# Optimization experiments

Hardware: AMD Instinct MI355X
Metric: run time of the kernel (lower is better)

Reference implementation:

```python
import jax, jax.numpy as jnp
import numpy as np
import math


def pos_enc_3d(h, w, d, c):
    # Faithful PositionalEncoding3D: channels = ceil(c/6)*2 (made even), sin/cos per axis.
    cpe = int(np.ceil(c / 6) * 2)
    if cpe % 2:
        cpe += 1
    inv_freq = 1.0 / (10000.0 ** (np.arange(0, cpe, 2, dtype=np.float32) / cpe))

    def axis_emb(n):
        s = np.arange(n, dtype=np.float32)[:, None] * inv_freq  # (n, cpe//2)
        return np.concatenate([np.sin(s), np.cos(s)], axis=-1)  # (n, cpe)

    ex = np.broadcast_to(axis_emb(h)[:, None, None, :], (h, w, d, cpe))
    ey = np.broadcast_to(axis_emb(w)[None, :, None, :], (h, w, d, cpe))
    ez = np.broadcast_to(axis_emb(d)[None, None, :, :], (h, w, d, cpe))
    emb = np.concatenate([ex, ey, ez], axis=-1)[..., :c]  # (h,w,d,c)
    return jnp.asarray(np.transpose(emb, (3, 0, 1, 2)))  # (c,h,w,d)


def conv3d(x, w, b):
    # x: (b,c,h,w,d), w: (o,i,3,3,3), padding=1
    y = jax.lax.conv_general_dilated(
        x, w, window_strides=(1, 1, 1), padding=[(1, 1)] * 3,
        dimension_numbers=('NCHWD', 'OIHWD', 'NCHWD'))
    return y + b[None, :, None, None, None]


def setup_inputs() -> dict:
    key = jax.random.key(0)
    ks = jax.random.split(key, 12)
    B, C, H, W, D = 2, 64, 16, 16, 16
    C8 = C // 8
    s_emb = 1.0 / math.sqrt(C)
    s_conv = 1.0 / math.sqrt(C * 27)
    return {
        'x': jax.random.normal(ks[0], (B, C, H, W, D), dtype=jnp.float32),
        'Wq': jax.random.normal(ks[1], (C, C), dtype=jnp.float32) * s_emb,
        'Wk': jax.random.normal(ks[2], (C, C), dtype=jnp.float32) * s_emb,
        'Wv': jax.random.normal(ks[3], (C, C), dtype=jnp.float32) * s_emb,
        'qw': jax.random.normal(ks[4], (C8, C, 3, 3, 3), dtype=jnp.float32) * s_conv,
        'qb': jax.random.normal(ks[5], (C8,), dtype=jnp.float32) * 0.01,
        'kw': jax.random.normal(ks[6], (C8, C, 3, 3, 3), dtype=jnp.float32) * s_conv,
        'kb': jax.random.normal(ks[7], (C8,), dtype=jnp.float32) * 0.01,
        'vw': jax.random.normal(ks[8], (C, C, 3, 3, 3), dtype=jnp.float32) * s_conv,
        'vb': jax.random.normal(ks[9], (C,), dtype=jnp.float32) * 0.01,
        'lam1': jax.random.normal(ks[10], (1,), dtype=jnp.float32) * 0.5,
        'lam2': jax.random.normal(ks[11], (1,), dtype=jnp.float32) * 0.5,
    }


def reference(x, Wq, Wk, Wv, qw, qb, kw, kb, vw, vb, lam1, lam2):
    b, c, h, w, d = x.shape
    n = h * w * d
    # NOTE: torch code does `x += pe` in-place inside SelfAttention, so the
    # PE-added x is also what GSA and the residual see.
    pe = pos_enc_3d(h, w, d, c)  # (c,h,w,d)
    x_pe = x + pe[None]

    # ---- SelfAttention (TSA) ----
    tok = x_pe.reshape(b, c, n).transpose(0, 2, 1)  # (b,n,c)
    Q = jnp.einsum('bnc,cd->bnd', tok, Wq)
    K = jnp.einsum('bnc,cd->bnd', tok, Wk)
    V = jnp.einsum('bnc,cd->bnd', tok, Wv)
    A = jax.nn.softmax(jnp.einsum('bic,bjc->bij', Q, K) / math.sqrt(c), axis=-1)
    tsa = jnp.einsum('bij,bjc->bic', A, V).transpose(0, 2, 1).reshape(b, c, h, w, d)

    # ---- GlobalSpatialAttention (GSA) ----
    M = conv3d(x_pe, qw, qb).reshape(b, c // 8, n)   # (b,c/8,n)
    Nk = conv3d(x_pe, kw, kb).reshape(b, c // 8, n)  # (b,c/8,n)
    Wv_ = conv3d(x_pe, vw, vb).reshape(b, c, n)      # (b,c,n)
    Bm = jax.nn.softmax(jnp.einsum('bci,bcj->bij', M, Nk), axis=-1)  # (b,n,n)
    gsa = jnp.einsum('bcj,bij->bci', Wv_, Bm).reshape(b, c, h, w, d)

    return lam1[0] * tsa + lam2[0] * gsa + x_pe
```

## Files before the change

kernel.cpp:

```cpp
#include <hip/hip_runtime.h>
#include <math.h>

#define BB 2
#define CC 64
#define NN 4096
#define CN (CC*NN)
#define NJ 8
#define NT ((NN/NJ)/64)

#define LOG2E 1.4426950408889634f
#define QSCALE 0.18033688011112042f

#define XT_ROWS 4097
#define WQKV_OFF (27*80*64)

typedef __attribute__((ext_vector_type(8))) short short8;
typedef __attribute__((ext_vector_type(4))) float float4v;
typedef unsigned short ushortT;

__device__ __forceinline__ ushortT f2bf(float x) {
    union { float f; unsigned u; } v; v.f = x;
    unsigned r = v.u + 0x7FFF + ((v.u >> 16) & 1);
    return (ushortT)(r >> 16);
}
__device__ __forceinline__ float bf2f(short s) {
    union { unsigned u; float f; } v;
    v.u = ((unsigned)(unsigned short)s) << 16;
    return v.f;
}
__device__ __forceinline__ unsigned pk2(float a, float b) {
    unsigned ua = __float_as_uint(a) + 0x8000u;
    unsigned ub = __float_as_uint(b) + 0x8000u;
    return __builtin_amdgcn_perm(ub, ua, 0x07060302);
}

__device__ __forceinline__ float pe_tab_val(int c, int pos) {
    int c2 = (c < 22) ? c : (c < 44) ? (c - 22) : (c - 44);
    int is_cos = (c2 >= 11);
    int k = c2 - (is_cos ? 11 : 0);
    float freq = exp2f(-1.2079738526863135f * (float)k);
    float arg = (float)pos * freq;
    return is_cos ? cosf(arg) : sinf(arg);
}

__global__ __launch_bounds__(256) void k_pre(const float* __restrict__ x,
                                             const float* __restrict__ qw,
                                             const float* __restrict__ kw,
                                             const float* __restrict__ vw,
                                             const float* __restrict__ Wq,
                                             const float* __restrict__ Wk,
                                             const float* __restrict__ Wv,
                                             float* __restrict__ xpe,
                                             ushortT* __restrict__ Xt,
                                             ushortT* __restrict__ Wr,
                                             ushortT* __restrict__ Qb,
                                             ushortT* __restrict__ Kb,
                                             ushortT* __restrict__ Vtb) {
    int blk = blockIdx.x, t = threadIdx.x;
    if (blk < 128) {
        __shared__ float sT[64][65];
        __shared__ float sPE[64][17];
        __shared__ ushortT sWt[64][72];
        __shared__ ushortT sVt[64][72];
        int b = blk >> 6, pos0 = (blk & 63) * 64;

        #pragma unroll
        for (int k = 0; k < 4; k++) {
            int e = t + k * 256;
            int c = e >> 4, coord = e & 15;
            sPE[c][coord] = pe_tab_val(c, coord);
        }
        __syncthreads();

        int pin = t & 63, cg0 = t >> 6;
        #pragma unroll
        for (int pass = 0; pass < 16; pass++) {
            int c = pass * 4 + cg0;
            int pos = pos0 + pin;
            int coord = (c < 22) ? (pos >> 8) : (c < 44) ? ((pos >> 4) & 15) : (pos & 15);
            size_t gi = (size_t)(b * 64 + c) * NN + pos;
            float v = x[gi] + sPE[c][coord];
            xpe[gi] = v;
            sT[c][pin] = v;
        }
        __syncthreads();

        {
            int icn = t & 63, pg = t >> 6;
            #pragma unroll
            for (int pass = 0; pass < 16; pass++) {
                int po = pass * 4 + pg;
                Xt[((size_t)b * XT_ROWS + pos0 + po + 1) * 64 + icn] = f2bf(sT[icn][po]);
            }
            if ((blk & 63) == 0 && t < 64)
                Xt[((size_t)b * XT_ROWS) * 64 + t] = 0;
        }

        int w = t >> 6, l = t & 63, lane15 = l & 15, q = l >> 4;
        int row = w * 16 + lane15;
        short8 a0, a1;
        {
            union { ushortT u[8]; short8 s; } t0, t1;
            #pragma unroll
            for (int e = 0; e < 8; e++) {
                t0.u[e] = f2bf(sT[q * 8 + e][row]);
                t1.u[e] = f2bf(sT[32 + q * 8 + e][row]);
            }
            a0 = t0.s; a1 = t1.s;
        }

        #pragma unroll
        for (int mat = 0; mat < 3; mat++) {
            const float* Wm = (mat == 0) ? Wq : (mat == 1) ? Wk : Wv;
            float sc = (mat == 0) ? QSCALE : 1.f;
            __syncthreads();
            #pragma unroll
            for (int p = 0; p < 4; p++) {
                int idx = t + p * 256;
                int c = idx >> 4, d4 = (idx & 15) * 4;
                float4 wv = *(const float4*)&Wm[c * 64 + d4];
                sWt[d4 + 0][c] = f2bf(wv.x * sc);
                sWt[d4 + 1][c] = f2bf(wv.y * sc);
                sWt[d4 + 2][c] = f2bf(wv.z * sc);
                sWt[d4 + 3][c] = f2bf(wv.w * sc);
            }
            __syncthreads();

            float4v acc[4];
            #pragma unroll
            for (int cg = 0; cg < 4; cg++) {
                const ushortT* wrow = &sWt[cg * 16 + lane15][0];
                short8 b0 = *(const short8*)(wrow + q * 8);
                short8 b1 = *(const short8*)(wrow + 32 + q * 8);
                float4v a = (float4v)0.f;
                a = __builtin_amdgcn_mfma_f32_16x16x32_bf16(a0, b0, a, 0, 0, 0);
                a = __builtin_amdgcn_mfma_f32_16x16x32_bf16(a1, b1, a, 0, 0, 0);
                acc[cg] = a;
            }
            if (mat < 2) {
                ushortT* o = (mat == 0) ? Qb : Kb;
                #pragma unroll
                for (int cg = 0; cg < 4; cg++)
                    #pragma unroll
                    for (int r = 0; r < 4; r++)
                        o[((size_t)(b * NN + pos0 + w * 16 + q * 4 + r)) * 64 + cg * 16 + lane15] = f2bf(acc[cg][r]);
            } else {
                #pragma unroll
                for (int cg = 0; cg < 4; cg++)
                    #pragma unroll
                    for (int r = 0; r < 4; r++)
                        sVt[cg * 16 + lane15][w * 16 + q * 4 + r] = f2bf(acc[cg][r]);
                __syncthreads();
                int c2 = t >> 2, seg = t & 3;
                short8 v0 = *(const short8*)&sVt[c2][seg * 16];
                short8 v1 = *(const short8*)&sVt[c2][seg * 16 + 8];
                size_t base = ((size_t)(b * 64 + c2)) * NN + pos0 + seg * 16;
                *(short8*)(Vtb + base) = v0;
                *(short8*)(Vtb + base + 8) = v1;
            }
        }
    } else {
        int idx = (blk - 128) * 256 + t;
        if (idx < WQKV_OFF) {
            int ic = idx & 63;
            int oc = (idx >> 6) % 80;
            int tap = idx / 5120;
            float v;
            if (oc < 8)       v = qw[(oc * 64 + ic) * 27 + tap] * LOG2E;
            else if (oc < 16) v = kw[((oc - 8) * 64 + ic) * 27 + tap];
            else              v = vw[((oc - 16) * 64 + ic) * 27 + tap];
            Wr[idx] = f2bf(v);
        }
    }
}

template<int IS_TSA>
__device__ __forceinline__ void stage_load(short8* kst, short8* vst,
                                           const ushortT* __restrict__ Km,
                                           const ushortT* __restrict__ Vt,
                                           int b, int jb, int t) {
    if (IS_TSA) {
        #pragma unroll
        for (int ps = 0; ps < 2; ps++) {
            int idx = ps * 256 + t, j = idx >> 3, g = idx & 7;
            kst[ps] = *(const short8*)(Km + ((size_t)(b * NN + jb + j)) * 64 + g * 8);
        }
    } else {
        if (t < 64)
            kst[0] = *(const short8*)(Km + ((size_t)(b * NN + jb + t)) * 8);
    }
    #pragma unroll
    for (int ps = 0; ps < 2; ps++) {
        int idx = ps * 256 + t, c = idx >> 3, gj = idx & 7;
        vst[ps] = *(const short8*)(Vt + ((size_t)(b * 64 + c)) * NN + jb + gj * 8);
    }
}

template<int IS_TSA>
__device__ __forceinline__ void stage_write(const short8* kst, const short8* vst,
                                            ushortT* sK, ushortT* sV, int t) {
    if (IS_TSA) {
        #pragma unroll
        for (int ps = 0; ps < 2; ps++) {
            int idx = ps * 256 + t, j = idx >> 3, g = idx & 7;
            *(short8*)(sK + j * 64 + ((g ^ (j & 7)) * 8)) = kst[ps];
        }
    } else {
        if (t < 64)
            *(short8*)(sK + t * 64 + ((t & 7) * 8)) = kst[0];
    }
    #pragma unroll
    for (int ps = 0; ps < 2; ps++) {
        int idx = ps * 256 + t, c = idx >> 3, gj = idx & 7;
        *(short8*)(sV + c * 64 + ((gj ^ (c & 7)) * 8)) = vst[ps];
    }
}

template<int IS_TSA>
__device__ __forceinline__ void flash_body(int it, int jc, int b, int t,
                                           const ushortT* __restrict__ Qm,
                                           const ushortT* __restrict__ Km,
                                           const ushortT* __restrict__ Vt,
                                           float* __restrict__ pM,
                                           float* __restrict__ pL,
                                           ushortT* __restrict__ pAcc,
                                           ushortT* __restrict__ sKb,
                                           ushortT* __restrict__ sVb,
                                           ushortT* __restrict__ sPall) {
    constexpr int KCH = IS_TSA ? 2 : 1;
    constexpr int DQ  = IS_TSA ? 64 : 8;
    int w = t >> 6, l = t & 63;
    int lane15 = l & 15, q = l >> 4;
    int i0a = it * 128 + w * 16;
    ushortT* myP = sPall + w * (16 * 64);

    short8 qf[2][KCH];
    #pragma unroll
    for (int si = 0; si < 2; si++) {
        const ushortT* qrow = Qm + ((size_t)(b * NN + i0a + si * 64 + lane15)) * DQ;
        if (IS_TSA) {
            qf[si][0] = *(const short8*)(qrow + q * 8);
            qf[si][1] = *(const short8*)(qrow + 32 + q * 8);
        } else {
            short8 z = (short8)0;
            if (q == 0) z = *(const short8*)qrow;
            qf[si][0] = z;
        }
    }

    float m_run[2] = {-3e38f, -3e38f}, Lacc[2] = {0.f, 0.f};
    float4v O[2][4];
    #pragma unroll
    for (int si = 0; si < 2; si++)
        #pragma unroll
        for (int cs = 0; cs < 4; cs++) O[si][cs] = (float4v)0.f;

    const int jbase0 = jc * (NN / NJ);

    short8 kst[2], vst[2];
    stage_load<IS_TSA>(kst, vst, Km, Vt, b, jbase0, t);
    stage_write<IS_TSA>(kst, vst, sKb, sVb, t);
    __syncthreads();

    for (int jt = 0; jt < NT; jt++) {
        int cur = jt & 1;
        ushortT* cK = sKb + cur * 4096;
        ushortT* cV = sVb + cur * 4096;
        bool more = (jt + 1 < NT);

        if (more) stage_load<IS_TSA>(kst, vst, Km, Vt, b, jbase0 + (jt + 1) * 64, t);

        short8 kf[4][KCH];
        #pragma unroll
        for (int sub = 0; sub < 4; sub++) {
            int jr = sub * 16 + lane15;
            if (IS_TSA) {
                kf[sub][0] = *(const short8*)(cK + jr * 64 + (((0 * 4 + q) ^ (lane15 & 7)) * 8));
                kf[sub][1] = *(const short8*)(cK + jr * 64 + (((1 * 4 + q) ^ (lane15 & 7)) * 8));
            } else {
                short8 z = (short8)0;
                if (q == 0) z = *(const short8*)(cK + jr * 64 + ((lane15 & 7) * 8));
                kf[sub][0] = z;
            }
        }

        float4v s[2][4];
        #pragma unroll
        for (int si = 0; si < 2; si++)
            #pragma unroll
            for (int sub = 0; sub < 4; sub++) {
                float4v acc = (float4v)0.f;
                #pragma unroll
                for (int kc = 0; kc < KCH; kc++)
                    acc = __builtin_amdgcn_mfma_f32_16x16x32_bf16(kf[sub][kc], qf[si][kc], acc, 0, 0, 0);
                s[si][sub] = acc;
            }

        short8 va[4], vbf[4];
        #pragma unroll
        for (int sub = 0; sub < 4; sub++) {
            int cr = sub * 16 + lane15;
            va[sub]  = *(const short8*)(cV + cr * 64 + ((q ^ (lane15 & 7)) * 8));
            vbf[sub] = *(const short8*)(cV + cr * 64 + (((4 + q) ^ (lane15 & 7)) * 8));
        }

        #pragma unroll
        for (int si = 0; si < 2; si++) {
            float tmax = fmaxf(fmaxf(fmaxf(s[si][0][0], s[si][0][1]), fmaxf(s[si][0][2], s[si][0][3])),
                               fmaxf(fmaxf(s[si][1][0], s[si][1][1]), fmaxf(s[si][1][2], s[si][1][3])));
            float tmax2 = fmaxf(fmaxf(fmaxf(s[si][2][0], s[si][2][1]), fmaxf(s[si][2][2], s[si][2][3])),
                                fmaxf(fmaxf(s[si][3][0], s[si][3][1]), fmaxf(s[si][3][2], s[si][3][3])));
            tmax = fmaxf(tmax, tmax2);
            tmax = fmaxf(tmax, __shfl_xor(tmax, 16));
            tmax = fmaxf(tmax, __shfl_xor(tmax, 32));
            float mnew = fmaxf(m_run[si], tmax);

            if (__any(mnew > m_run[si])) {
                float corr = exp2f(m_run[si] - mnew);
                Lacc[si] *= corr;
                float c0 = __shfl(corr, q * 4 + 0);
                float c1 = __shfl(corr, q * 4 + 1);
                float c2 = __shfl(corr, q * 4 + 2);
                float c3 = __shfl(corr, q * 4 + 3);
                #pragma unroll
                for (int cs = 0; cs < 4; cs++) {
                    O[si][cs][0] *= c0; O[si][cs][1] *= c1;
                    O[si][cs][2] *= c2; O[si][cs][3] *= c3;
                }
            }
            m_run[si] = mnew;

            #pragma unroll
            for (int sub = 0; sub < 4; sub++) {
                float p0 = exp2f(s[si][sub][0] - mnew);
                float p1 = exp2f(s[si][sub][1] - mnew);
                float p2 = exp2f(s[si][sub][2] - mnew);
                float p3 = exp2f(s[si][sub][3] - mnew);
                Lacc[si] += (p0 + p1) + (p2 + p3);
                unsigned lo = pk2(p0, p1), hi = pk2(p2, p3);
                int g = sub * 2 + (q >> 1);
                unsigned* wp = (unsigned*)(myP + lane15 * 64 + ((g ^ (lane15 & 7)) * 8) + (q & 1) * 4);
                wp[0] = lo; wp[1] = hi;
            }

            short8 pf0 = *(const short8*)(myP + lane15 * 64 + (((0 * 4 + q) ^ (lane15 & 7)) * 8));
            short8 pf1 = *(const short8*)(myP + lane15 * 64 + (((1 * 4 + q) ^ (lane15 & 7)) * 8));

            #pragma unroll
            for (int sub = 0; sub < 4; sub++) {
                O[si][sub] = __builtin_amdgcn_mfma_f32_16x16x32_bf16(pf0, va[sub], O[si][sub], 0, 0, 0);
                O[si][sub] = __builtin_amdgcn_mfma_f32_16x16x32_bf16(pf1, vbf[sub], O[si][sub], 0, 0, 0);
            }
        }

        if (more)
            stage_write<IS_TSA>(kst, vst, sKb + (cur ^ 1) * 4096, sVb + (cur ^ 1) * 4096, t);
        __syncthreads();
    }

    #pragma unroll
    for (int si = 0; si < 2; si++) {
        size_t base = (size_t)(b * NJ + jc) * NN + i0a + si * 64;
        float Ls = Lacc[si];
        Ls += __shfl_xor(Ls, 16);
        Ls += __shfl_xor(Ls, 32);
        if (q == 0) {
            pL[base + lane15] = Ls;
            pM[base + lane15] = m_run[si];
        }
        #pragma unroll
        for (int cs = 0; cs < 4; cs++)
            #pragma unroll
            for (int r = 0; r < 4; r++)
                pAcc[(base + q * 4 + r) * 64 + cs * 16 + lane15] = f2bf(O[si][cs][r]);
    }
}

__device__ __forceinline__ void reduce_set(const float* __restrict__ pM,
                                           const float* __restrict__ pL,
                                           const ushortT* __restrict__ pAcc,
                                           int b, int n, int seg, float* v) {
    float mv[NJ], M = -3e38f;
    #pragma unroll
    for (int jcc = 0; jcc < NJ; jcc++) {
        mv[jcc] = pM[(size_t)(b * NJ + jcc) * NN + n];
        M = fmaxf(M, mv[jcc]);
    }
    float L = 0.f;
    #pragma unroll
    for (int e = 0; e < 8; e++) v[e] = 0.f;
    #pragma unroll
    for (int jcc = 0; jcc < NJ; jcc++) {
        size_t rb = (size_t)(b * NJ + jcc) * NN + n;
        float wgt = exp2f(mv[jcc] - M);
        L += pL[rb] * wgt;
        short8 x0 = *(const short8*)(pAcc + rb * 64 + seg * 8);
        #pragma unroll
        for (int e = 0; e < 8; e++) v[e] += wgt * bf2f(x0[e]);
    }
    float invL = 1.f / L;
    #pragma unroll
    for (int e = 0; e < 8; e++) v[e] *= invL;
}

__global__ __launch_bounds__(256, 3) void k_tsacv(const ushortT* __restrict__ Qb,
                                                  const ushortT* __restrict__ Kb,
                                                  const ushortT* __restrict__ Vtb,
                                                  const ushortT* __restrict__ Xt,
                                                  const ushortT* __restrict__ Wr,
                                                  const float* __restrict__ qb,
                                                  const float* __restrict__ kb,
                                                  const float* __restrict__ vb,
                                                  ushortT* __restrict__ Mt,
                                                  ushortT* __restrict__ Nt,
                                                  ushortT* __restrict__ Wvt,
                                                  float* __restrict__ pMt, float* __restrict__ pLt,
                                                  ushortT* __restrict__ pAccT) {
    __shared__ ushortT sm[20480];
    int bx = blockIdx.x, t = threadIdx.x;
    if (bx >= 128) {
        int fb = bx - 128;
        int it = fb & 31, jc = (fb >> 5) & 7, b = fb >> 8;
        flash_body<1>(it, jc, b, t, Qb, Kb, Vtb, pMt, pLt, pAccT,
                      sm, sm + 8192, sm + 16384);
    } else {
        int cv = bx;
        int tile = cv & 63, b = cv >> 6;
        int w = t >> 6, l = t & 63, lane15 = l & 15, q = l >> 4;
        int pos0 = tile * 64 + w * 16;
        const ushortT* xb = Xt + (size_t)b * XT_ROWS * 64;
        int pos = pos0 + lane15;
        int dz = pos & 15, wy = (pos >> 4) & 15, hx = pos >> 8;

        ushortT* sW = sm;

        float4v accA[5], accB[5];
        #pragma unroll
        for (int o = 0; o < 5; o++) { accA[o] = (float4v)0.f; accB[o] = (float4v)0.f; }

        short8 ws[3];
        auto ldW = [&](int tap) {
            #pragma unroll
            for (int c3 = 0; c3 < 3; c3++) {
                int idx = t + c3 * 256;
                if (idx < 640)
                    ws[c3] = *(const short8*)(Wr + (size_t)tap * 5120 + idx * 8);
            }
        };
        auto wrW = [&](ushortT* buf) {
            #pragma unroll
            for (int c3 = 0; c3 < 3; c3++) {
                int idx = t + c3 * 256;
                if (idx < 640) {
                    int row = idx >> 3, g = idx & 7;
                    *(short8*)(buf + row * 64 + ((g ^ (row & 7)) * 8)) = ws[c3];
                }
            }
        };

        ldW(0);
        wrW(sW);
        __syncthreads();

        #pragma unroll
        for (int tap = 0; tap < 27; tap++) {
            const int dh = tap / 9 - 1, dw = (tap / 3) % 3 - 1, dd = tap % 3 - 1;
            const int shift = dh * 256 + dw * 16 + dd;
            ushortT* cW = sW + (tap & 1) * 5120;
            bool more = (tap + 1 < 27);

            if (more) ldW(tap + 1);

            bool ok = ((unsigned)(hx + dh) < 16u) &&
                      ((unsigned)(wy + dw) < 16u) &&
                      ((unsigned)(dz + dd) < 16u);
            int row = ok ? (pos + shift + 1) : 0;
            const ushortT* xrow = xb + (size_t)row * 64 + q * 8;
            short8 b0 = *(const short8*)xrow;
            short8 b1 = *(const short8*)(xrow + 32);

            #pragma unroll
            for (int o = 0; o < 5; o++) {
                int wr2 = o * 16 + lane15;
                short8 a0 = *(const short8*)(cW + wr2 * 64 + ((q ^ (lane15 & 7)) * 8));
                short8 a1 = *(const short8*)(cW + wr2 * 64 + (((4 + q) ^ (lane15 & 7)) * 8));
                accA[o] = __builtin_amdgcn_mfma_f32_16x16x32_bf16(a0, b0, accA[o], 0, 0, 0);
                accB[o] = __builtin_amdgcn_mfma_f32_16x16x32_bf16(a1, b1, accB[o], 0, 0, 0);
            }

            if (more) wrW(sW + ((tap + 1) & 1) * 5120);
            __syncthreads();
        }

        #pragma unroll
        for (int o = 0; o < 5; o++) {
            float4v accT = accA[o] + accB[o];
            if (o == 0) {
                #pragma unroll
                for (int r = 0; r < 4; r++) {
                    int ol = q * 4 + r;
                    float v = accT[r];
                    if (ol < 8)
                        Mt[((size_t)(b * NN + pos)) * 8 + ol] = f2bf(v + qb[ol] * LOG2E);
                    else
                        Nt[((size_t)(b * NN + pos)) * 8 + (ol - 8)] = f2bf(v + kb[ol - 8]);
                }
            } else {
                #pragma unroll
                for (int r = 0; r < 4; r++) {
                    int oc = (o - 1) * 16 + q * 4 + r;
                    Wvt[((size_t)(b * 64 + oc)) * NN + pos] = f2bf(accT[r] + vb[oc]);
                }
            }
        }
    }
}

__global__ __launch_bounds__(256, 3) void k_gsa(const ushortT* __restrict__ Mtb,
                                                const ushortT* __restrict__ Ntb,
                                                const ushortT* __restrict__ Wvtb,
                                                float* __restrict__ pMg, float* __restrict__ pLg,
                                                ushortT* __restrict__ pAccG,
                                                const float* __restrict__ pMt,
                                                const float* __restrict__ pLt,
                                                const ushortT* __restrict__ pAccT,
                                                const float* __restrict__ xpe,
                                                const float* __restrict__ lam1,
                                                float* __restrict__ out) {
    __shared__ ushortT sm[20480];
    int bx = blockIdx.x, t = threadIdx.x;
    if (bx < 512) {
        int it = bx & 31, jc = (bx >> 5) & 7, b = bx >> 8;
        flash_body<0>(it, jc, b, t, Mtb, Ntb, Wvtb, pMg, pLg, pAccG,
                      sm, sm + 8192, sm + 16384);
    } else {
        int rb = bx - 512;
        int b = rb >> 7, n0 = (rb & 127) * 32;
        float (*sT_)[65] = (float(*)[65])sm;
        int pp = t >> 3, seg = t & 7, n = n0 + pp;

        float vt[8];
        reduce_set(pMt, pLt, pAccT, b, n, seg, vt);
        #pragma unroll
        for (int e = 0; e < 8; e++) sT_[pp][seg * 8 + e] = vt[e];
        __syncthreads();

        int c = t >> 2, ns = (t & 3) * 8;
        float la1 = lam1[0];
        size_t ob = ((size_t)(b * 64 + c)) * NN + n0 + ns;
        const float* xp = xpe + ob;
        #pragma unroll
        for (int j = 0; j < 8; j += 4) {
            float4 ov;
            ov.x = la1 * sT_[ns + j + 0][c] + xp[j + 0];
            ov.y = la1 * sT_[ns + j + 1][c] + xp[j + 1];
            ov.z = la1 * sT_[ns + j + 2][c] + xp[j + 2];
            ov.w = la1 * sT_[ns + j + 3][c] + xp[j + 3];
            *(float4*)(out + ob + j) = ov;
        }
    }
}

__global__ __launch_bounds__(256) void k_reduce_g(const float* __restrict__ pMg,
                                                  const float* __restrict__ pLg,
                                                  const ushortT* __restrict__ pAccG,
                                                  const float* __restrict__ lam2,
                                                  float* __restrict__ out) {
    __shared__ float sG[32][65];
    int t = threadIdx.x;
    int b = blockIdx.y;
    int n0 = blockIdx.x * 32;
    int pp = t >> 3, seg = t & 7;
    int n = n0 + pp;

    float vg[8];
    reduce_set(pMg, pLg, pAccG, b, n, seg, vg);
    #pragma unroll
    for (int e = 0; e < 8; e++) sG[pp][seg * 8 + e] = vg[e];
    __syncthreads();

    int c = t >> 2, ns = (t & 3) * 8;
    float la2 = lam2[0];
    size_t ob = ((size_t)(b * 64 + c)) * NN + n0 + ns;
    #pragma unroll
    for (int j = 0; j < 8; j += 4) {
        float4 cur = *(const float4*)(out + ob + j);
        cur.x += la2 * sG[ns + j + 0][c];
        cur.y += la2 * sG[ns + j + 1][c];
        cur.z += la2 * sG[ns + j + 2][c];
        cur.w += la2 * sG[ns + j + 3][c];
        *(float4*)(out + ob + j) = cur;
    }
}

extern "C" void kernel_launch(void* const* d_in, const int* in_sizes, int n_in,
                              void* d_out, int out_size, void* d_ws, size_t ws_size,
                              hipStream_t stream) {
    const float* x    = (const float*)d_in[0];
    const float* Wq   = (const float*)d_in[1];
    const float* Wk   = (const float*)d_in[2];
    const float* Wv   = (const float*)d_in[3];
    const float* qw   = (const float*)d_in[4];
    const float* qb   = (const float*)d_in[5];
    const float* kw   = (const float*)d_in[6];
    const float* kb   = (const float*)d_in[7];
    const float* vw   = (const float*)d_in[8];
    const float* vb   = (const float*)d_in[9];
    const float* lam1 = (const float*)d_in[10];
    const float* lam2 = (const float*)d_in[11];
    float* out = (float*)d_out;

    char* W = (char*)d_ws;
    float*   xpe   = (float*)(W);
    ushortT* Qb    = (ushortT*)(W + (2u << 20));
    ushortT* Kb    = (ushortT*)(W + (3u << 20));
    ushortT* Vtb   = (ushortT*)(W + (4u << 20));
    ushortT* Mtb   = (ushortT*)(W + (5u << 20));
    ushortT* Ntb   = (ushortT*)(W + (5u << 20) + (1u << 17));
    ushortT* Wvtb  = (ushortT*)(W + (5u << 20) + (2u << 17));
    ushortT* Xt    = (ushortT*)(W + (6u << 20) + (2u << 17));
    ushortT* Wr    = (ushortT*)(W + (7u << 20) + (1u << 19));
    float*   pLt   = (float*)(W + (8u << 20));
    float*   pLg   = (float*)(W + (8u << 20) + (1u << 18));
    float*   pMt   = (float*)(W + (8u << 20) + (2u << 18));
    float*   pMg   = (float*)(W + (8u << 20) + (3u << 18));
    ushortT* pAccT = (ushortT*)(W + (9u << 20));
    ushortT* pAccG = (ushortT*)(W + (17u << 20));

    k_pre<<<dim3(128 + WQKV_OFF / 256), dim3(256), 0, stream>>>(
        x, qw, kw, vw, Wq, Wk, Wv, xpe, Xt, Wr, Qb, Kb, Vtb);
    k_tsacv<<<dim3(128 + 32 * NJ * BB), dim3(256), 0, stream>>>(
        Qb, Kb, Vtb, Xt, Wr, qb, kb, vb, Mtb, Ntb, Wvtb, pMt, pLt, pAccT);
    k_gsa<<<dim3(512 + 256), dim3(256), 0, stream>>>(
        Mtb, Ntb, Wvtb, pMg, pLg, pAccG, pMt, pLt, pAccT, xpe, lam1, out);
    k_reduce_g<<<dim3(NN / 32, BB), dim3(256), 0, stream>>>(
        pMg, pLg, pAccG, lam2, out);
}
```

Baseline: 132.8 us.

## Vectorize global stores, lazy softmax rescale, and prefetch conv input rows

Stores to Xt, Q/K and the partial attention accumulator now go through shared memory, so each thread writes 16-byte short8 chunks instead of scattered 2-byte values. The online softmax skips rescaling unless the tile max exceeds the running max by more than a threshold of 8 (log2 units), which removes most correction multiplies and exp2 calls. The conv loop prefetches the next tap's input rows into registers alongside the weight prefetch, hiding global load latency. The costs are extra barriers and shared-memory round trips, plus bf16 P values that can reach up to 2^8 before a rescale happens.

After: 131.7 us. About the same (-0.8%).

```diff
diff --git a/kernel.cpp b/kernel.cpp
--- a/kernel.cpp
+++ b/kernel.cpp
@@ -10,6 +10,7 @@
 
 #define LOG2E 1.4426950408889634f
 #define QSCALE 0.18033688011112042f
+#define RESC_THR 8.0f
 
 #define XT_ROWS 4097
 #define WQKV_OFF (27*80*64)
@@ -86,11 +87,14 @@
         __syncthreads();
 
         {
-            int icn = t & 63, pg = t >> 6;
-            #pragma unroll
-            for (int pass = 0; pass < 16; pass++) {
-                int po = pass * 4 + pg;
-                Xt[((size_t)b * XT_ROWS + pos0 + po + 1) * 64 + icn] = f2bf(sT[icn][po]);
+            int po = t & 63, cg = t >> 6;
+            #pragma unroll
+            for (int half = 0; half < 2; half++) {
+                int c0 = cg * 8 + half * 32;
+                union { ushortT u[8]; short8 s; } pk_;
+                #pragma unroll
+                for (int e = 0; e < 8; e++) pk_.u[e] = f2bf(sT[c0 + e][po]);
+                *(short8*)(Xt + ((size_t)b * XT_ROWS + pos0 + po + 1) * 64 + c0) = pk_.s;
             }
             if ((blk & 63) == 0 && t < 64)
                 Xt[((size_t)b * XT_ROWS) * 64 + t] = 0;
@@ -138,12 +142,19 @@
                 acc[cg] = a;
             }
             if (mat < 2) {
-                ushortT* o = (mat == 0) ? Qb : Kb;
                 #pragma unroll
                 for (int cg = 0; cg < 4; cg++)
                     #pragma unroll
                     for (int r = 0; r < 4; r++)
-                        o[((size_t)(b * NN + pos0 + w * 16 + q * 4 + r)) * 64 + cg * 16 + lane15] = f2bf(acc[cg][r]);
+                        sVt[w * 16 + q * 4 + r][cg * 16 + lane15] = f2bf(acc[cg][r]);
+                __syncthreads();
+                ushortT* o = (mat == 0) ? Qb : Kb;
+                int pl = t >> 2, sg = t & 3;
+                short8 v0 = *(const short8*)&sVt[pl][sg * 16];
+                short8 v1 = *(const short8*)&sVt[pl][sg * 16 + 8];
+                size_t bq = ((size_t)(b * NN + pos0 + pl)) * 64 + sg * 16;
+                *(short8*)(o + bq) = v0;
+                *(short8*)(o + bq + 8) = v1;
             } else {
                 #pragma unroll
                 for (int cg = 0; cg < 4; cg++)
@@ -313,9 +324,9 @@
             tmax = fmaxf(tmax, tmax2);
             tmax = fmaxf(tmax, __shfl_xor(tmax, 16));
             tmax = fmaxf(tmax, __shfl_xor(tmax, 32));
-            float mnew = fmaxf(m_run[si], tmax);
-
-            if (__any(mnew > m_run[si])) {
+
+            if (!__all(tmax <= m_run[si] + RESC_THR)) {
+                float mnew = fmaxf(m_run[si], tmax);
                 float corr = exp2f(m_run[si] - mnew);
                 Lacc[si] *= corr;
                 float c0 = __shfl(corr, q * 4 + 0);
@@ -327,15 +338,16 @@
                     O[si][cs][0] *= c0; O[si][cs][1] *= c1;
                     O[si][cs][2] *= c2; O[si][cs][3] *= c3;
                 }
-            }
-            m_run[si] = mnew;
+                m_run[si] = mnew;
+            }
+            float mcur = m_run[si];
 
             #pragma unroll
             for (int sub = 0; sub < 4; sub++) {
-                float p0 = exp2f(s[si][sub][0] - mnew);
-                float p1 = exp2f(s[si][sub][1] - mnew);
-                float p2 = exp2f(s[si][sub][2] - mnew);
-                float p3 = exp2f(s[si][sub][3] - mnew);
+                float p0 = exp2f(s[si][sub][0] - mcur);
+                float p1 = exp2f(s[si][sub][1] - mcur);
+                float p2 = exp2f(s[si][sub][2] - mcur);
+                float p3 = exp2f(s[si][sub][3] - mcur);
                 Lacc[si] += (p0 + p1) + (p2 + p3);
                 unsigned lo = pk2(p0, p1), hi = pk2(p2, p3);
                 int g = sub * 2 + (q >> 1);
@@ -369,10 +381,20 @@
             pM[base + lane15] = m_run[si];
         }
         #pragma unroll
-        for (int cs = 0; cs < 4; cs++)
-            #pragma unroll
-            for (int r = 0; r < 4; r++)
-                pAcc[(base + q * 4 + r) * 64 + cs * 16 + lane15] = f2bf(O[si][cs][r]);
+        for (int cs = 0; cs < 4; cs++) {
+            int g = cs * 2 + (lane15 >> 3);
+            #pragma unroll
+            for (int r = 0; r < 4; r++) {
+                int rr = q * 4 + r;
+                myP[rr * 64 + ((g ^ (rr & 7)) * 8) + (lane15 & 7)] = f2bf(O[si][cs][r]);
+            }
+        }
+        int rrow = l >> 2, rs2 = (l & 3) * 2;
+        short8 ov0 = *(const short8*)(myP + rrow * 64 + ((rs2 ^ (rrow & 7)) * 8));
+        short8 ov1 = *(const short8*)(myP + rrow * 64 + (((rs2 + 1) ^ (rrow & 7)) * 8));
+        size_t gb = (base + rrow) * 64 + (l & 3) * 16;
+        *(short8*)(pAcc + gb) = ov0;
+        *(short8*)(pAcc + gb + 8) = ov1;
     }
 }
 
@@ -457,39 +479,43 @@
                 }
             }
         };
-
-        ldW(0);
-        wrW(sW);
-        __syncthreads();
-
-        #pragma unroll
-        for (int tap = 0; tap < 27; tap++) {
-            const int dh = tap / 9 - 1, dw = (tap / 3) % 3 - 1, dd = tap % 3 - 1;
-            const int shift = dh * 256 + dw * 16 + dd;
-            ushortT* cW = sW + (tap & 1) * 5120;
-            bool more = (tap + 1 < 27);
-
-            if (more) ldW(tap + 1);
-
+        short8 xc0, xc1, xn0, xn1;
+        auto ldX = [&](int tap, short8& o0, short8& o1) {
+            int dh = tap / 9 - 1, dw = (tap / 3) % 3 - 1, dd = tap % 3 - 1;
+            int shift = dh * 256 + dw * 16 + dd;
             bool ok = ((unsigned)(hx + dh) < 16u) &&
                       ((unsigned)(wy + dw) < 16u) &&
                       ((unsigned)(dz + dd) < 16u);
             int row = ok ? (pos + shift + 1) : 0;
             const ushortT* xrow = xb + (size_t)row * 64 + q * 8;
-            short8 b0 = *(const short8*)xrow;
-            short8 b1 = *(const short8*)(xrow + 32);
+            o0 = *(const short8*)xrow;
+            o1 = *(const short8*)(xrow + 32);
+        };
+
+        ldW(0);
+        ldX(0, xc0, xc1);
+        wrW(sW);
+        __syncthreads();
+
+        #pragma unroll
+        for (int tap = 0; tap < 27; tap++) {
+            ushortT* cW = sW + (tap & 1) * 5120;
+            bool more = (tap + 1 < 27);
+
+            if (more) { ldW(tap + 1); ldX(tap + 1, xn0, xn1); }
 
             #pragma unroll
             for (int o = 0; o < 5; o++) {
                 int wr2 = o * 16 + lane15;
                 short8 a0 = *(const short8*)(cW + wr2 * 64 + ((q ^ (lane15 & 7)) * 8));
                 short8 a1 = *(const short8*)(cW + wr2 * 64 + (((4 + q) ^ (lane15 & 7)) * 8));
-                accA[o] = __builtin_amdgcn_mfma_f32_16x16x32_bf16(a0, b0, accA[o], 0, 0, 0);
-                accB[o] = __builtin_amdgcn_mfma_f32_16x16x32_bf16(a1, b1, accB[o], 0, 0, 0);
+                accA[o] = __builtin_amdgcn_mfma_f32_16x16x32_bf16(a0, xc0, accA[o], 0, 0, 0);
+                accB[o] = __builtin_amdgcn_mfma_f32_16x16x32_bf16(a1, xc1, accB[o], 0, 0, 0);
             }
 
             if (more) wrW(sW + ((tap + 1) & 1) * 5120);
             __syncthreads();
+            xc0 = xn0; xc1 = xn1;
         }
 
         #pragma unroll
```
